# Performance work log

Measured on AMD Instinct MI355X. Metric: run time of the kernel, lower is better.

## Reference

```python
import jax, jax.numpy as jnp
import numpy as np

DIM = 64
D_STATE = 64          # = d_inner // 2, required for consistency
D_CONV = 4
EXPAND = 2
D_INNER = EXPAND * DIM  # 128
BATCH = 2
SEQ = 2048


def setup_inputs() -> dict:
    key = jax.random.key(0)
    k0, k1, k2, k3, k4, k5 = jax.random.split(key, 6)
    return {
        "x": jax.random.normal(k0, (BATCH, SEQ, DIM), jnp.float32),
        # torch nn.Linear weight layout: (out_features, in_features)
        "W_proj": jax.random.normal(k1, (3 * D_INNER, DIM), jnp.float32) / np.sqrt(DIM),
        # torch depthwise Conv1d weight layout: (d_inner, 1, d_conv)
        "conv_w": jax.random.normal(k2, (D_INNER, 1, D_CONV), jnp.float32) / np.sqrt(D_CONV),
        "conv_b": jax.random.normal(k3, (D_INNER,), jnp.float32) * 0.01,
        # negative A so exp(delta * rowsum(A)) is a stable decay (<1)
        "A": -jnp.abs(jax.random.normal(k4, (D_STATE, D_STATE), jnp.float32)) * 0.1,
        "D": jax.random.normal(k5, (D_INNER,), jnp.float32),
    }


def _scan_dir(A_bar, bx, reverse):
    # A_bar, bx: (B, L, n, d). Linear recurrence h_t = A_t * h_{t-1} + bx_t.
    A_t = jnp.moveaxis(A_bar, 1, 0)  # (L, B, n, d)
    b_t = jnp.moveaxis(bx, 1, 0)
    h0 = jnp.zeros(A_t.shape[1:], A_t.dtype)

    def step(h, inp):
        a, b = inp
        h = a * h + b
        return h, h

    _, hs = jax.lax.scan(step, h0, (A_t, b_t), reverse=reverse)
    return jnp.moveaxis(hs, 0, 1)  # (B, L, n, d)


def _forward(x, W_proj, conv_w, conv_b, A, D):
    d_inner = D.shape[0]
    n = A.shape[0]
    k = conv_w.shape[-1]

    xp = x @ W_proj.T                                   # (B, L, 3*d_inner)
    x_c_in, delta_raw, BC = jnp.split(xp, [d_inner, 2 * d_inner], axis=-1)

    # causal depthwise conv1d (torch pads d_conv-1 both sides then slices [:L])
    xc = jnp.swapaxes(x_c_in, 1, 2)                     # (B, d, L)
    xc = jax.lax.conv_general_dilated(
        xc, conv_w, window_strides=(1,), padding=[(k - 1, 0)],
        dimension_numbers=("NCH", "OIH", "NCH"), feature_group_count=d_inner)
    xc = xc + conv_b[None, :, None]
    x_conv = jnp.swapaxes(xc, 1, 2)                     # (B, L, d_inner)

    delta = jax.nn.sigmoid(delta_raw)                   # (B, L, d_inner)
    B_in, C_in = BC[..., :n], BC[..., n:]               # (B, L, n) each

    a = A.sum(axis=1)                                   # 'ij->i' contraction, (n,)
    # A_bar[b,l,n,d] = exp(delta[b,l,d] * a[n])
    A_bar = jnp.exp(delta[:, :, None, :] * a[None, None, :, None])
    # (delta*B) * x, broadcast into (B, L, n, d)
    bx = (delta * x_conv)[:, :, None, :] * B_in[..., None]

    h = _scan_dir(A_bar, bx, False) + _scan_dir(A_bar, bx, True)  # (B,L,n,d)

    y = jnp.einsum("blnd,bln->bld", h, C_in) + D * x_conv
    return y


def reference(x, W_proj, conv_w, conv_b, A, D):
    return _forward(x, W_proj, conv_w, conv_b, A, D)
```

## Files before the change

### kernel.cpp

```cpp
#include <hip/hip_runtime.h>

#define BB   2
#define TT   2048
#define DIN  128
#define NS   64
#define CL   16
#define NC   128
#define NSUP 16
#define SUPW 8
#define NP   32
#define L2E  1.4426950408889634f

#if __has_builtin(__builtin_amdgcn_exp2f)
__device__ __forceinline__ float fexp2(float x) { return __builtin_amdgcn_exp2f(x); }
#else
__device__ __forceinline__ float fexp2(float x) { return exp2f(x); }
#endif

__device__ __forceinline__ unsigned int f2bf(float f) {
  unsigned int u = __float_as_uint(f);
  u += 0x7FFFu + ((u >> 16) & 1u);
  return u >> 16;
}
__device__ __forceinline__ unsigned int packbf2(float a, float b) {
  return f2bf(a) | (f2bf(b) << 16);
}
__device__ __forceinline__ float bflo(unsigned int u) { return __uint_as_float(u << 16); }
__device__ __forceinline__ float bfhi(unsigned int u) { return __uint_as_float(u & 0xFFFF0000u); }

__global__ __launch_bounds__(128) void k_proj(
    const float* __restrict__ x, const float* __restrict__ W,
    const float* __restrict__ A,
    float* __restrict__ xcin, float* __restrict__ delta,
    float* __restrict__ Bb, float* __restrict__ Cb, float* __restrict__ a2g) {
  __shared__ float xs[128 * 65];
  int tile = blockIdx.x, rg = blockIdx.y, tid = threadIdx.x;
  int base = tile * 128;
  const float4* __restrict__ x4 = (const float4*)(x + (size_t)base * 64);
  for (int i = tid; i < 128 * 16; i += 128) {
    float4 v = x4[i];
    int row = i >> 4, c4 = (i & 15) << 2;
    xs[row * 65 + c4 + 0] = v.x;
    xs[row * 65 + c4 + 1] = v.y;
    xs[row * 65 + c4 + 2] = v.z;
    xs[row * 65 + c4 + 3] = v.w;
  }
  if (tile == 0 && rg == 0 && tid < NS) {
    float s = 0.f;
    for (int m = 0; m < NS; ++m) s += A[tid * NS + m];
    a2g[tid] = s * L2E;
  }
  __syncthreads();
  float xr[64];
#pragma unroll
  for (int k = 0; k < 64; ++k) xr[k] = xs[tid * 65 + k];
  int bt = base + tid;
#pragma unroll 4
  for (int rr = 0; rr < 16; ++rr) {
    int r = rg * 16 + rr;
    const float* __restrict__ wrow = W + r * 64;
    float a0 = 0.f, a1 = 0.f, a2 = 0.f, a3 = 0.f;
#pragma unroll
    for (int k = 0; k < 64; k += 4) {
      a0 = fmaf(xr[k + 0], wrow[k + 0], a0);
      a1 = fmaf(xr[k + 1], wrow[k + 1], a1);
      a2 = fmaf(xr[k + 2], wrow[k + 2], a2);
      a3 = fmaf(xr[k + 3], wrow[k + 3], a3);
    }
    float acc = (a0 + a1) + (a2 + a3);
    if (r < 128) {
      xcin[(size_t)bt * DIN + r] = acc;
    } else if (r < 256) {
      delta[(size_t)bt * DIN + (r - 128)] = 1.f / (1.f + fexp2(-acc * L2E));
    } else if (r < 320) {
      Bb[(size_t)bt * NS + (r - 256)] = acc;
    } else {
      Cb[(size_t)bt * NS + (r - 320)] = acc;
    }
  }
}

__global__ __launch_bounds__(1024) void k_scan1(
    const float* __restrict__ xcin, const float* __restrict__ delta,
    const float* __restrict__ Bb, const float* __restrict__ a2g,
    const float* __restrict__ cw, const float* __restrict__ cb,
    unsigned int* __restrict__ hendP, float* __restrict__ sumd) {
  __shared__ float xcs[(CL + 3) * DIN];
  __shared__ float des[CL * DIN];
  __shared__ float Bs[CL * NS];
  int c = blockIdx.x, b = blockIdx.y;
  int tid = threadIdx.x;
  int d = tid & 127;
  int g = __builtin_amdgcn_readfirstlane(tid >> 7);
  int t0 = c * CL;
  {
    const float* __restrict__ xcB = xcin + (size_t)b * TT * DIN;
    for (int i = tid; i < (CL + 3) * 32; i += 1024) {
      int row = i >> 5, c4 = i & 31;
      int t = t0 - 3 + row;
      float4 v = make_float4(0.f, 0.f, 0.f, 0.f);
      if (t >= 0) v = ((const float4*)(xcB + (size_t)t * DIN))[c4];
      ((float4*)xcs)[i] = v;
    }
    if (tid < CL * 32)
      ((float4*)des)[tid] = ((const float4*)(delta + (size_t)(b * TT + t0) * DIN))[tid];
    if (tid < CL * 16)
      ((float4*)Bs)[tid] = ((const float4*)(Bb + (size_t)(b * TT + t0) * NS))[tid];
  }
  float cw0 = cw[d * 4 + 0], cw1 = cw[d * 4 + 1], cw2 = cw[d * 4 + 2], cw3 = cw[d * 4 + 3];
  float cbd = cb[d];
  int nb = g * 8;
  float a2r[8];
#pragma unroll
  for (int j = 0; j < 8; ++j) a2r[j] = a2g[nb + j];
  __syncthreads();
  float hf[8], hr[8], Pp[8];
#pragma unroll
  for (int j = 0; j < 8; ++j) { hf[j] = 0.f; hr[j] = 0.f; Pp[j] = 1.f; }
  float sd = 0.f;
  float w0 = xcs[0 * DIN + d], w1 = xcs[1 * DIN + d], w2 = xcs[2 * DIN + d];
#pragma unroll
  for (int i = 0; i < CL; ++i) {
    float w3 = xcs[(i + 3) * DIN + d];
    float xconv = fmaf(cw0, w0, fmaf(cw1, w1, fmaf(cw2, w2, fmaf(cw3, w3, cbd))));
    float de = des[i * DIN + d];
    sd += de;
    float dxv = de * xconv;
#pragma unroll
    for (int jq = 0; jq < 2; ++jq) {
      float4 bq = *(const float4*)&Bs[i * NS + nb + jq * 4];
      float b0 = dxv * bq.x, b1 = dxv * bq.y, b2 = dxv * bq.z, b3 = dxv * bq.w;
      float e0 = fexp2(de * a2r[jq * 4 + 0]);
      float e1 = fexp2(de * a2r[jq * 4 + 1]);
      float e2 = fexp2(de * a2r[jq * 4 + 2]);
      float e3 = fexp2(de * a2r[jq * 4 + 3]);
      hf[jq * 4 + 0] = fmaf(e0, hf[jq * 4 + 0], b0);
      hr[jq * 4 + 0] = fmaf(Pp[jq * 4 + 0], b0, hr[jq * 4 + 0]); Pp[jq * 4 + 0] *= e0;
      hf[jq * 4 + 1] = fmaf(e1, hf[jq * 4 + 1], b1);
      hr[jq * 4 + 1] = fmaf(Pp[jq * 4 + 1], b1, hr[jq * 4 + 1]); Pp[jq * 4 + 1] *= e1;
      hf[jq * 4 + 2] = fmaf(e2, hf[jq * 4 + 2], b2);
      hr[jq * 4 + 2] = fmaf(Pp[jq * 4 + 2], b2, hr[jq * 4 + 2]); Pp[jq * 4 + 2] *= e2;
      hf[jq * 4 + 3] = fmaf(e3, hf[jq * 4 + 3], b3);
      hr[jq * 4 + 3] = fmaf(Pp[jq * 4 + 3], b3, hr[jq * 4 + 3]); Pp[jq * 4 + 3] *= e3;
    }
    w0 = w1; w1 = w2; w2 = w3;
  }
  size_t h0 = (((size_t)(0 * NC + c) * BB + b) * NP + (nb >> 1)) * DIN + d;
  size_t h1 = (((size_t)(1 * NC + c) * BB + b) * NP + (nb >> 1)) * DIN + d;
#pragma unroll
  for (int jp = 0; jp < 4; ++jp) {
    hendP[h0 + (size_t)jp * DIN] = packbf2(hf[2 * jp], hf[2 * jp + 1]);
    hendP[h1 + (size_t)jp * DIN] = packbf2(hr[2 * jp], hr[2 * jp + 1]);
  }
  if (g == 0) sumd[(c * BB + b) * DIN + d] = sd;
}

__global__ __launch_bounds__(512) void k_comb2A(
    const unsigned int* __restrict__ hendP, unsigned int* __restrict__ hinLP,
    const float* __restrict__ sumd, const float* __restrict__ a2g,
    float* __restrict__ S, float* __restrict__ sumdS,
    float* __restrict__ sumdPf, float* __restrict__ sumdPr) {
  int idx = blockIdx.x * 512 + threadIdx.x;
  int dd = idx & 127;
  int np = (idx >> 7) & 31;
  int sp = (idx >> 12) & 15;
  int bd = idx >> 16;
  int b = bd >> 1, dir = bd & 1;
  int n0 = 2 * np, n1 = 2 * np + 1;
  float a2n0 = a2g[n0], a2n1 = a2g[n1];
  float sd[SUPW];
  unsigned int hv[SUPW];
#pragma unroll
  for (int k = 0; k < SUPW; ++k) {
    int kk = dir ? (SUPW - 1 - k) : k;
    int cc = sp * SUPW + kk;
    sd[k] = sumd[(cc * BB + b) * DIN + dd];
    hv[k] = hendP[(((size_t)(dir * NC + cc) * BB + b) * NP + np) * DIN + dd];
  }
  if (np == 0) {
    float running = 0.f;
#pragma unroll
    for (int k = 0; k < SUPW; ++k) {
      int kk = dir ? (SUPW - 1 - k) : k;
      int cc = sp * SUPW + kk;
      if (dir) sumdPr[(cc * BB + b) * DIN + dd] = running;
      else     sumdPf[(cc * BB + b) * DIN + dd] = running;
      running += sd[k];
    }
    if (dir == 0) sumdS[(sp * BB + b) * DIN + dd] = running;
  }
  float c0 = 0.f, c1 = 0.f;
#pragma unroll
  for (int k = 0; k < SUPW; ++k) {
    int kk = dir ? (SUPW - 1 - k) : k;
    int cc = sp * SUPW + kk;
    hinLP[(((size_t)(dir * NC + cc) * BB + b) * NP + np) * DIN + dd] = packbf2(c0, c1);
    float e0 = fexp2(a2n0 * sd[k]);
    float e1 = fexp2(a2n1 * sd[k]);
    c0 = fmaf(e0, c0, bflo(hv[k]));
    c1 = fmaf(e1, c1, bfhi(hv[k]));
  }
  size_t sb = ((((size_t)dir * NSUP + sp) * BB + b) * NS + n0) * DIN + dd;
  S[sb] = c0;
  S[sb + (size_t)DIN] = c1;
}

__global__ __launch_bounds__(256) void k_comb2B(
    const float* __restrict__ S, const float* __restrict__ sumdS,
    const float* __restrict__ a2g, float* __restrict__ Csup) {
  int idx = blockIdx.x * 256 + threadIdx.x;
  int dd = idx & 127;
  int n = (idx >> 7) & 63;
  int bd = idx >> 13;
  int b = bd >> 1, dir = bd & 1;
  float a2n = a2g[n];
  float sdS[NSUP], Sv[NSUP];
#pragma unroll
  for (int sp = 0; sp < NSUP; ++sp) {
    sdS[sp] = sumdS[(sp * BB + b) * DIN + dd];
    Sv[sp] = S[((((size_t)dir * NSUP + sp) * BB + b) * NS + n) * DIN + dd];
  }
  float carry = 0.f;
#pragma unroll
  for (int k = 0; k < NSUP; ++k) {
    int sp = dir ? (NSUP - 1 - k) : k;
    Csup[((((size_t)dir * NSUP + sp) * BB + b) * NS + n) * DIN + dd] = carry;
    carry = fmaf(fexp2(a2n * sdS[sp]), carry, Sv[sp]);
  }
}

__global__ __launch_bounds__(1024) void k_scan2(
    const float* __restrict__ xcin, const float* __restrict__ delta,
    const float* __restrict__ Bb, const float* __restrict__ Cb,
    const float* __restrict__ a2g, const float* __restrict__ cw,
    const float* __restrict__ cb, const float* __restrict__ Dp,
    const unsigned int* __restrict__ hinLP, const float* __restrict__ Csup,
    const float* __restrict__ sumdPf, const float* __restrict__ sumdPr,
    float* __restrict__ out) {
  __shared__ float yred[8][CL][DIN];
  int c = blockIdx.x, b = blockIdx.y;
  int tid = threadIdx.x;
  int d = tid & 127;
  int g = __builtin_amdgcn_readfirstlane(tid >> 7);
  int dir = g >> 2;
  int nb = (g & 3) * 16;
  float cw0 = cw[d * 4 + 0], cw1 = cw[d * 4 + 1], cw2 = cw[d * 4 + 2], cw3 = cw[d * 4 + 3];
  float cbd = cb[d];
  float Dd = Dp[d];
  float a2r[16];
#pragma unroll
  for (int j = 0; j < 16; ++j) a2r[j] = a2g[nb + j];
  int sp = c >> 3;
  float Sloc = dir ? sumdPr[(c * BB + b) * DIN + d] : sumdPf[(c * BB + b) * DIN + d];
  float h[16];
  size_t hb0 = (((size_t)(dir * NC + c) * BB + b) * NP + (nb >> 1)) * DIN + d;
  size_t sb0 = ((((size_t)dir * NSUP + sp) * BB + b) * NS + nb) * DIN + d;
#pragma unroll
  for (int jp = 0; jp < 8; ++jp) {
    unsigned int u = hinLP[hb0 + (size_t)jp * DIN];
    float pe0 = fexp2(a2r[2 * jp] * Sloc);
    float pe1 = fexp2(a2r[2 * jp + 1] * Sloc);
    h[2 * jp]     = fmaf(pe0, Csup[sb0 + (size_t)(2 * jp) * DIN], bflo(u));
    h[2 * jp + 1] = fmaf(pe1, Csup[sb0 + (size_t)(2 * jp + 1) * DIN], bfhi(u));
  }
  int t0 = c * CL;
  const float* __restrict__ xcB = xcin + (size_t)b * TT * DIN + d;
  const float* __restrict__ deB = delta + (size_t)b * TT * DIN + d;
  const float* __restrict__ BbB = Bb + (size_t)b * TT * NS + nb;
  const float* __restrict__ CbB = Cb + (size_t)b * TT * NS + nb;
  bool addD = (g == 0);
  float w0, w1, w2, w3;
  if (dir == 0) {
    int t = t0;
    w0 = (t - 3 >= 0) ? xcB[(t - 3) * DIN] : 0.f;
    w1 = (t - 2 >= 0) ? xcB[(t - 2) * DIN] : 0.f;
    w2 = (t - 1 >= 0) ? xcB[(t - 1) * DIN] : 0.f;
    w3 = xcB[t * DIN];
#pragma unroll
    for (int i = 0; i < CL; ++i) {
      float xconv = fmaf(cw0, w0, fmaf(cw1, w1, fmaf(cw2, w2, fmaf(cw3, w3, cbd))));
      float de = deB[t * DIN];
      float dxv = de * xconv;
      float yv = addD ? Dd * xconv : 0.f;
#pragma unroll
      for (int jq = 0; jq < 4; ++jq) {
        float4 bq = *(const float4*)&BbB[t * NS + jq * 4];
        float4 cq = *(const float4*)&CbB[t * NS + jq * 4];
        float e0 = fexp2(de * a2r[jq * 4 + 0]);
        h[jq * 4 + 0] = fmaf(e0, h[jq * 4 + 0], dxv * bq.x); yv = fmaf(h[jq * 4 + 0], cq.x, yv);
        float e1 = fexp2(de * a2r[jq * 4 + 1]);
        h[jq * 4 + 1] = fmaf(e1, h[jq * 4 + 1], dxv * bq.y); yv = fmaf(h[jq * 4 + 1], cq.y, yv);
        float e2 = fexp2(de * a2r[jq * 4 + 2]);
        h[jq * 4 + 2] = fmaf(e2, h[jq * 4 + 2], dxv * bq.z); yv = fmaf(h[jq * 4 + 2], cq.z, yv);
        float e3 = fexp2(de * a2r[jq * 4 + 3]);
        h[jq * 4 + 3] = fmaf(e3, h[jq * 4 + 3], dxv * bq.w); yv = fmaf(h[jq * 4 + 3], cq.w, yv);
      }
      yred[g][i][d] = yv;
      if (i < CL - 1) { ++t; w0 = w1; w1 = w2; w2 = w3; w3 = xcB[t * DIN]; }
    }
  } else {
    int t = t0 + CL - 1;
    w3 = xcB[t * DIN];
    w2 = xcB[(t - 1) * DIN];
    w1 = xcB[(t - 2) * DIN];
    w0 = xcB[(t - 3) * DIN];
#pragma unroll
    for (int i = 0; i < CL; ++i) {
      float xconv = fmaf(cw0, w0, fmaf(cw1, w1, fmaf(cw2, w2, fmaf(cw3, w3, cbd))));
      float de = deB[t * DIN];
      float dxv = de * xconv;
      float yv = 0.f;
#pragma unroll
      for (int jq = 0; jq < 4; ++jq) {
        float4 bq = *(const float4*)&BbB[t * NS + jq * 4];
        float4 cq = *(const float4*)&CbB[t * NS + jq * 4];
        float e0 = fexp2(de * a2r[jq * 4 + 0]);
        h[jq * 4 + 0] = fmaf(e0, h[jq * 4 + 0], dxv * bq.x); yv = fmaf(h[jq * 4 + 0], cq.x, yv);
        float e1 = fexp2(de * a2r[jq * 4 + 1]);
        h[jq * 4 + 1] = fmaf(e1, h[jq * 4 + 1], dxv * bq.y); yv = fmaf(h[jq * 4 + 1], cq.y, yv);
        float e2 = fexp2(de * a2r[jq * 4 + 2]);
        h[jq * 4 + 2] = fmaf(e2, h[jq * 4 + 2], dxv * bq.z); yv = fmaf(h[jq * 4 + 2], cq.z, yv);
        float e3 = fexp2(de * a2r[jq * 4 + 3]);
        h[jq * 4 + 3] = fmaf(e3, h[jq * 4 + 3], dxv * bq.w); yv = fmaf(h[jq * 4 + 3], cq.w, yv);
      }
      yred[g][i][d] = yv;
      if (i < CL - 1) { --t; w3 = w2; w2 = w1; w1 = w0; w0 = (t - 3 >= 0) ? xcB[(t - 3) * DIN] : 0.f; }
    }
  }
  __syncthreads();
#pragma unroll
  for (int k = 0; k < 2; ++k) {
    int p = k * 1024 + tid;
    int i = p >> 7, d2 = p & 127;
    int ir = CL - 1 - i;
    float sf = (yred[0][i][d2] + yred[1][i][d2]) + (yred[2][i][d2] + yred[3][i][d2]);
    float sr = (yred[4][ir][d2] + yred[5][ir][d2]) + (yred[6][ir][d2] + yred[7][ir][d2]);
    out[((size_t)b * TT + t0 + i) * DIN + d2] = sf + sr;
  }
}

extern "C" void kernel_launch(void* const* d_in, const int* in_sizes, int n_in,
                              void* d_out, int out_size, void* d_ws, size_t ws_size,
                              hipStream_t stream) {
  const float* x  = (const float*)d_in[0];
  const float* W  = (const float*)d_in[1];
  const float* cw = (const float*)d_in[2];
  const float* cb = (const float*)d_in[3];
  const float* A  = (const float*)d_in[4];
  const float* Dp = (const float*)d_in[5];
  float* out = (float*)d_out;

  float* ws = (float*)d_ws;
  float* xcin   = ws;
  float* delta  = xcin + 524288;
  float* Bbuf   = delta + 524288;
  float* Cbuf   = Bbuf + 262144;
  float* a2g    = Cbuf + 262144;
  float* sumd   = a2g + 128;
  float* sumdPf = sumd + 32768;
  float* sumdPr = sumdPf + 32768;
  float* sumdS  = sumdPr + 32768;
  float* Sb     = sumdS + 4096;
  float* Csup   = Sb + 524288;
  unsigned int* hendP = (unsigned int*)(Csup + 524288);
  unsigned int* hinLP = hendP + 2097152;

  hipLaunchKernelGGL(k_proj,   dim3(32, 24), dim3(128), 0, stream,
                     x, W, A, xcin, delta, Bbuf, Cbuf, a2g);
  hipLaunchKernelGGL(k_scan1,  dim3(NC, BB), dim3(1024), 0, stream,
                     xcin, delta, Bbuf, a2g, cw, cb, hendP, sumd);
  hipLaunchKernelGGL(k_comb2A, dim3(512), dim3(512), 0, stream,
                     hendP, hinLP, sumd, a2g, Sb, sumdS, sumdPf, sumdPr);
  hipLaunchKernelGGL(k_comb2B, dim3(128), dim3(256), 0, stream,
                     Sb, sumdS, a2g, Csup);
  hipLaunchKernelGGL(k_scan2,  dim3(NC, BB), dim3(1024), 0, stream,
                     xcin, delta, Bbuf, Cbuf, a2g, cw, cb, Dp, hinLP, Csup,
                     sumdPf, sumdPr, out);
}
```

Baseline: 62.96 us.

## Recompute intra-superchunk carry in scan2 instead of storing hinLP; split proj tiles

Drops the hinLP buffer that k_comb2A wrote and k_scan2 read. k_scan2 now rebuilds the within-superchunk incoming state itself by walking up to seven preceding chunk-end states from hendP, then adds the superchunk carry. This saves a large bf16 write and read pass but adds redundant exp and FMA work and serial loads inside scan2, with uneven work across chunks. Separately, k_proj now uses 64-row tiles with each half of the block computing 8 output rows, which doubles the grid.

```diff
diff --git a/kernel.cpp b/kernel.cpp
--- a/kernel.cpp
+++ b/kernel.cpp
@@ -33,11 +33,11 @@
     const float* __restrict__ A,
     float* __restrict__ xcin, float* __restrict__ delta,
     float* __restrict__ Bb, float* __restrict__ Cb, float* __restrict__ a2g) {
-  __shared__ float xs[128 * 65];
+  __shared__ float xs[64 * 65];
   int tile = blockIdx.x, rg = blockIdx.y, tid = threadIdx.x;
-  int base = tile * 128;
+  int base = tile * 64;
   const float4* __restrict__ x4 = (const float4*)(x + (size_t)base * 64);
-  for (int i = tid; i < 128 * 16; i += 128) {
+  for (int i = tid; i < 64 * 16; i += 128) {
     float4 v = x4[i];
     int row = i >> 4, c4 = (i & 15) << 2;
     xs[row * 65 + c4 + 0] = v.x;
@@ -51,13 +51,14 @@
     a2g[tid] = s * L2E;
   }
   __syncthreads();
+  int tl = tid & 63, half = tid >> 6;
   float xr[64];
 #pragma unroll
-  for (int k = 0; k < 64; ++k) xr[k] = xs[tid * 65 + k];
-  int bt = base + tid;
+  for (int k = 0; k < 64; ++k) xr[k] = xs[tl * 65 + k];
+  int bt = base + tl;
 #pragma unroll 4
-  for (int rr = 0; rr < 16; ++rr) {
-    int r = rg * 16 + rr;
+  for (int rr = 0; rr < 8; ++rr) {
+    int r = rg * 16 + half * 8 + rr;
     const float* __restrict__ wrow = W + r * 64;
     float a0 = 0.f, a1 = 0.f, a2 = 0.f, a3 = 0.f;
 #pragma unroll
@@ -156,7 +157,7 @@
 }
 
 __global__ __launch_bounds__(512) void k_comb2A(
-    const unsigned int* __restrict__ hendP, unsigned int* __restrict__ hinLP,
+    const unsigned int* __restrict__ hendP,
     const float* __restrict__ sumd, const float* __restrict__ a2g,
     float* __restrict__ S, float* __restrict__ sumdS,
     float* __restrict__ sumdPf, float* __restrict__ sumdPr) {
@@ -192,9 +193,6 @@
   float c0 = 0.f, c1 = 0.f;
 #pragma unroll
   for (int k = 0; k < SUPW; ++k) {
-    int kk = dir ? (SUPW - 1 - k) : k;
-    int cc = sp * SUPW + kk;
-    hinLP[(((size_t)(dir * NC + cc) * BB + b) * NP + np) * DIN + dd] = packbf2(c0, c1);
     float e0 = fexp2(a2n0 * sd[k]);
     float e1 = fexp2(a2n1 * sd[k]);
     c0 = fmaf(e0, c0, bflo(hv[k]));
@@ -234,7 +232,8 @@
     const float* __restrict__ Bb, const float* __restrict__ Cb,
     const float* __restrict__ a2g, const float* __restrict__ cw,
     const float* __restrict__ cb, const float* __restrict__ Dp,
-    const unsigned int* __restrict__ hinLP, const float* __restrict__ Csup,
+    const unsigned int* __restrict__ hendP, const float* __restrict__ sumd,
+    const float* __restrict__ Csup,
     const float* __restrict__ sumdPf, const float* __restrict__ sumdPr,
     float* __restrict__ out) {
   __shared__ float yred[8][CL][DIN];
@@ -253,15 +252,40 @@
   int sp = c >> 3;
   float Sloc = dir ? sumdPr[(c * BB + b) * DIN + d] : sumdPf[(c * BB + b) * DIN + d];
   float h[16];
-  size_t hb0 = (((size_t)(dir * NC + c) * BB + b) * NP + (nb >> 1)) * DIN + d;
+#pragma unroll
+  for (int j = 0; j < 16; ++j) h[j] = 0.f;
+  if (dir == 0) {
+    for (int kc = sp * 8; kc < c; ++kc) {
+      float sdv = sumd[(kc * BB + b) * DIN + d];
+      size_t hb = (((size_t)(0 * NC + kc) * BB + b) * NP + (nb >> 1)) * DIN + d;
+#pragma unroll
+      for (int jp = 0; jp < 8; ++jp) {
+        unsigned int u = hendP[hb + (size_t)jp * DIN];
+        float e0 = fexp2(a2r[2 * jp] * sdv);
+        float e1 = fexp2(a2r[2 * jp + 1] * sdv);
+        h[2 * jp]     = fmaf(e0, h[2 * jp], bflo(u));
+        h[2 * jp + 1] = fmaf(e1, h[2 * jp + 1], bfhi(u));
+      }
+    }
+  } else {
+    for (int kc = sp * 8 + 7; kc > c; --kc) {
+      float sdv = sumd[(kc * BB + b) * DIN + d];
+      size_t hb = (((size_t)(1 * NC + kc) * BB + b) * NP + (nb >> 1)) * DIN + d;
+#pragma unroll
+      for (int jp = 0; jp < 8; ++jp) {
+        unsigned int u = hendP[hb + (size_t)jp * DIN];
+        float e0 = fexp2(a2r[2 * jp] * sdv);
+        float e1 = fexp2(a2r[2 * jp + 1] * sdv);
+        h[2 * jp]     = fmaf(e0, h[2 * jp], bflo(u));
+        h[2 * jp + 1] = fmaf(e1, h[2 * jp + 1], bfhi(u));
+      }
+    }
+  }
   size_t sb0 = ((((size_t)dir * NSUP + sp) * BB + b) * NS + nb) * DIN + d;
 #pragma unroll
-  for (int jp = 0; jp < 8; ++jp) {
-    unsigned int u = hinLP[hb0 + (size_t)jp * DIN];
-    float pe0 = fexp2(a2r[2 * jp] * Sloc);
-    float pe1 = fexp2(a2r[2 * jp + 1] * Sloc);
-    h[2 * jp]     = fmaf(pe0, Csup[sb0 + (size_t)(2 * jp) * DIN], bflo(u));
-    h[2 * jp + 1] = fmaf(pe1, Csup[sb0 + (size_t)(2 * jp + 1) * DIN], bfhi(u));
+  for (int j = 0; j < 16; ++j) {
+    float pe = fexp2(a2r[j] * Sloc);
+    h[j] = fmaf(pe, Csup[sb0 + (size_t)j * DIN], h[j]);
   }
   int t0 = c * CL;
   const float* __restrict__ xcB = xcin + (size_t)b * TT * DIN + d;
@@ -363,17 +387,16 @@
   float* Sb     = sumdS + 4096;
   float* Csup   = Sb + 524288;
   unsigned int* hendP = (unsigned int*)(Csup + 524288);
-  unsigned int* hinLP = hendP + 2097152;
-
-  hipLaunchKernelGGL(k_proj,   dim3(32, 24), dim3(128), 0, stream,
+
+  hipLaunchKernelGGL(k_proj,   dim3(64, 24), dim3(128), 0, stream,
                      x, W, A, xcin, delta, Bbuf, Cbuf, a2g);
   hipLaunchKernelGGL(k_scan1,  dim3(NC, BB), dim3(1024), 0, stream,
                      xcin, delta, Bbuf, a2g, cw, cb, hendP, sumd);
   hipLaunchKernelGGL(k_comb2A, dim3(512), dim3(512), 0, stream,
-                     hendP, hinLP, sumd, a2g, Sb, sumdS, sumdPf, sumdPr);
+                     hendP, sumd, a2g, Sb, sumdS, sumdPf, sumdPr);
   hipLaunchKernelGGL(k_comb2B, dim3(128), dim3(256), 0, stream,
                      Sb, sumdS, a2g, Csup);
   hipLaunchKernelGGL(k_scan2,  dim3(NC, BB), dim3(1024), 0, stream,
-                     xcin, delta, Bbuf, Cbuf, a2g, cw, cb, Dp, hinLP, Csup,
+                     xcin, delta, Bbuf, Cbuf, a2g, cw, cb, Dp, hendP, sumd, Csup,
                      sumdPf, sumdPr, out);
 }
```

New measurement: 67.41 us. 7.1% more time.

## Fuse two-level chunk carry combine into one kernel writing final carries

Applied to the files above, without the earlier changes.

Merges the two combine kernels into one block-per-(batch,dir,state-pair) kernel. It computes superchunk partial carries, runs the cross-superchunk scan in shared memory, then writes fully resolved bf16 initial states per chunk. The second scan kernel therefore no longer reads Csup and the prefix sums or evaluates extra exponentials at start. This removes one launch and several intermediate global buffers. The cost is only 128 blocks and a serial 16-step section run by one warp group, plus re-quantising the combined state to bf16.

```diff
diff --git a/kernel.cpp b/kernel.cpp
--- a/kernel.cpp
+++ b/kernel.cpp
@@ -155,77 +155,67 @@
   if (g == 0) sumd[(c * BB + b) * DIN + d] = sd;
 }
 
-__global__ __launch_bounds__(512) void k_comb2A(
-    const unsigned int* __restrict__ hendP, unsigned int* __restrict__ hinLP,
-    const float* __restrict__ sumd, const float* __restrict__ a2g,
-    float* __restrict__ S, float* __restrict__ sumdS,
-    float* __restrict__ sumdPf, float* __restrict__ sumdPr) {
-  int idx = blockIdx.x * 512 + threadIdx.x;
-  int dd = idx & 127;
-  int np = (idx >> 7) & 31;
-  int sp = (idx >> 12) & 15;
-  int bd = idx >> 16;
-  int b = bd >> 1, dir = bd & 1;
-  int n0 = 2 * np, n1 = 2 * np + 1;
-  float a2n0 = a2g[n0], a2n1 = a2g[n1];
-  float sd[SUPW];
-  unsigned int hv[SUPW];
-#pragma unroll
-  for (int k = 0; k < SUPW; ++k) {
-    int kk = dir ? (SUPW - 1 - k) : k;
-    int cc = sp * SUPW + kk;
-    sd[k] = sumd[(cc * BB + b) * DIN + dd];
-    hv[k] = hendP[(((size_t)(dir * NC + cc) * BB + b) * NP + np) * DIN + dd];
-  }
-  if (np == 0) {
-    float running = 0.f;
+__global__ __launch_bounds__(1024) void k_comb(
+    const unsigned int* __restrict__ hendP, const float* __restrict__ sumd,
+    const float* __restrict__ a2g, unsigned int* __restrict__ hinP) {
+  __shared__ float S0[NSUP][DIN], S1[NSUP][DIN];
+  __shared__ float sdS[NSUP][DIN];
+  __shared__ float C0[NSUP][DIN], C1[NSUP][DIN];
+  int bid = blockIdx.x;
+  int np = bid & 31;
+  int dirb = bid >> 5;
+  int dir = dirb & 1, b = dirb >> 1;
+  int tid = threadIdx.x;
+  int d = tid & 127;
+  int sl = __builtin_amdgcn_readfirstlane(tid >> 7);
+  float a2n0 = a2g[2 * np], a2n1 = a2g[2 * np + 1];
+  float hinLo0[2][SUPW], hinLo1[2][SUPW], pfLoc[2][SUPW];
+#pragma unroll
+  for (int ss = 0; ss < 2; ++ss) {
+    int sp = sl + ss * 8;
+    float c0 = 0.f, c1 = 0.f, pf = 0.f;
 #pragma unroll
     for (int k = 0; k < SUPW; ++k) {
-      int kk = dir ? (SUPW - 1 - k) : k;
-      int cc = sp * SUPW + kk;
-      if (dir) sumdPr[(cc * BB + b) * DIN + dd] = running;
-      else     sumdPf[(cc * BB + b) * DIN + dd] = running;
-      running += sd[k];
-    }
-    if (dir == 0) sumdS[(sp * BB + b) * DIN + dd] = running;
-  }
-  float c0 = 0.f, c1 = 0.f;
-#pragma unroll
-  for (int k = 0; k < SUPW; ++k) {
-    int kk = dir ? (SUPW - 1 - k) : k;
-    int cc = sp * SUPW + kk;
-    hinLP[(((size_t)(dir * NC + cc) * BB + b) * NP + np) * DIN + dd] = packbf2(c0, c1);
-    float e0 = fexp2(a2n0 * sd[k]);
-    float e1 = fexp2(a2n1 * sd[k]);
-    c0 = fmaf(e0, c0, bflo(hv[k]));
-    c1 = fmaf(e1, c1, bfhi(hv[k]));
-  }
-  size_t sb = ((((size_t)dir * NSUP + sp) * BB + b) * NS + n0) * DIN + dd;
-  S[sb] = c0;
-  S[sb + (size_t)DIN] = c1;
-}
-
-__global__ __launch_bounds__(256) void k_comb2B(
-    const float* __restrict__ S, const float* __restrict__ sumdS,
-    const float* __restrict__ a2g, float* __restrict__ Csup) {
-  int idx = blockIdx.x * 256 + threadIdx.x;
-  int dd = idx & 127;
-  int n = (idx >> 7) & 63;
-  int bd = idx >> 13;
-  int b = bd >> 1, dir = bd & 1;
-  float a2n = a2g[n];
-  float sdS[NSUP], Sv[NSUP];
-#pragma unroll
-  for (int sp = 0; sp < NSUP; ++sp) {
-    sdS[sp] = sumdS[(sp * BB + b) * DIN + dd];
-    Sv[sp] = S[((((size_t)dir * NSUP + sp) * BB + b) * NS + n) * DIN + dd];
-  }
-  float carry = 0.f;
-#pragma unroll
-  for (int k = 0; k < NSUP; ++k) {
-    int sp = dir ? (NSUP - 1 - k) : k;
-    Csup[((((size_t)dir * NSUP + sp) * BB + b) * NS + n) * DIN + dd] = carry;
-    carry = fmaf(fexp2(a2n * sdS[sp]), carry, Sv[sp]);
+      int cc = sp * SUPW + (dir ? (SUPW - 1 - k) : k);
+      float sdv = sumd[(cc * BB + b) * DIN + d];
+      unsigned int hv = hendP[(((size_t)(dir * NC + cc) * BB + b) * NP + np) * DIN + d];
+      hinLo0[ss][k] = c0; hinLo1[ss][k] = c1; pfLoc[ss][k] = pf;
+      float e0 = fexp2(a2n0 * sdv);
+      float e1 = fexp2(a2n1 * sdv);
+      c0 = fmaf(e0, c0, bflo(hv));
+      c1 = fmaf(e1, c1, bfhi(hv));
+      pf += sdv;
+    }
+    S0[sp][d] = c0; S1[sp][d] = c1; sdS[sp][d] = pf;
+  }
+  __syncthreads();
+  if (sl == 0) {
+    float c0 = 0.f, c1 = 0.f;
+#pragma unroll
+    for (int k = 0; k < NSUP; ++k) {
+      int sp = dir ? (NSUP - 1 - k) : k;
+      C0[sp][d] = c0; C1[sp][d] = c1;
+      float sv = sdS[sp][d];
+      float e0 = fexp2(a2n0 * sv);
+      float e1 = fexp2(a2n1 * sv);
+      c0 = fmaf(e0, c0, S0[sp][d]);
+      c1 = fmaf(e1, c1, S1[sp][d]);
+    }
+  }
+  __syncthreads();
+#pragma unroll
+  for (int ss = 0; ss < 2; ++ss) {
+    int sp = sl + ss * 8;
+    float cs0 = C0[sp][d], cs1 = C1[sp][d];
+#pragma unroll
+    for (int k = 0; k < SUPW; ++k) {
+      int cc = sp * SUPW + (dir ? (SUPW - 1 - k) : k);
+      float pe0 = fexp2(a2n0 * pfLoc[ss][k]);
+      float pe1 = fexp2(a2n1 * pfLoc[ss][k]);
+      float v0 = fmaf(pe0, cs0, hinLo0[ss][k]);
+      float v1 = fmaf(pe1, cs1, hinLo1[ss][k]);
+      hinP[(((size_t)(dir * NC + cc) * BB + b) * NP + np) * DIN + d] = packbf2(v0, v1);
+    }
   }
 }
 
@@ -234,8 +224,7 @@
     const float* __restrict__ Bb, const float* __restrict__ Cb,
     const float* __restrict__ a2g, const float* __restrict__ cw,
     const float* __restrict__ cb, const float* __restrict__ Dp,
-    const unsigned int* __restrict__ hinLP, const float* __restrict__ Csup,
-    const float* __restrict__ sumdPf, const float* __restrict__ sumdPr,
+    const unsigned int* __restrict__ hinP,
     float* __restrict__ out) {
   __shared__ float yred[8][CL][DIN];
   int c = blockIdx.x, b = blockIdx.y;
@@ -250,18 +239,13 @@
   float a2r[16];
 #pragma unroll
   for (int j = 0; j < 16; ++j) a2r[j] = a2g[nb + j];
-  int sp = c >> 3;
-  float Sloc = dir ? sumdPr[(c * BB + b) * DIN + d] : sumdPf[(c * BB + b) * DIN + d];
   float h[16];
   size_t hb0 = (((size_t)(dir * NC + c) * BB + b) * NP + (nb >> 1)) * DIN + d;
-  size_t sb0 = ((((size_t)dir * NSUP + sp) * BB + b) * NS + nb) * DIN + d;
 #pragma unroll
   for (int jp = 0; jp < 8; ++jp) {
-    unsigned int u = hinLP[hb0 + (size_t)jp * DIN];
-    float pe0 = fexp2(a2r[2 * jp] * Sloc);
-    float pe1 = fexp2(a2r[2 * jp + 1] * Sloc);
-    h[2 * jp]     = fmaf(pe0, Csup[sb0 + (size_t)(2 * jp) * DIN], bflo(u));
-    h[2 * jp + 1] = fmaf(pe1, Csup[sb0 + (size_t)(2 * jp + 1) * DIN], bfhi(u));
+    unsigned int u = hinP[hb0 + (size_t)jp * DIN];
+    h[2 * jp]     = bflo(u);
+    h[2 * jp + 1] = bfhi(u);
   }
   int t0 = c * CL;
   const float* __restrict__ xcB = xcin + (size_t)b * TT * DIN + d;
@@ -357,23 +341,15 @@
   float* Cbuf   = Bbuf + 262144;
   float* a2g    = Cbuf + 262144;
   float* sumd   = a2g + 128;
-  float* sumdPf = sumd + 32768;
-  float* sumdPr = sumdPf + 32768;
-  float* sumdS  = sumdPr + 32768;
-  float* Sb     = sumdS + 4096;
-  float* Csup   = Sb + 524288;
-  unsigned int* hendP = (unsigned int*)(Csup + 524288);
-  unsigned int* hinLP = hendP + 2097152;
-
-  hipLaunchKernelGGL(k_proj,   dim3(32, 24), dim3(128), 0, stream,
+  unsigned int* hendP = (unsigned int*)(sumd + 32768);
+  unsigned int* hinP  = hendP + 2097152;
+
+  hipLaunchKernelGGL(k_proj,  dim3(32, 24), dim3(128), 0, stream,
                      x, W, A, xcin, delta, Bbuf, Cbuf, a2g);
-  hipLaunchKernelGGL(k_scan1,  dim3(NC, BB), dim3(1024), 0, stream,
+  hipLaunchKernelGGL(k_scan1, dim3(NC, BB), dim3(1024), 0, stream,
                      xcin, delta, Bbuf, a2g, cw, cb, hendP, sumd);
-  hipLaunchKernelGGL(k_comb2A, dim3(512), dim3(512), 0, stream,
-                     hendP, hinLP, sumd, a2g, Sb, sumdS, sumdPf, sumdPr);
-  hipLaunchKernelGGL(k_comb2B, dim3(128), dim3(256), 0, stream,
-                     Sb, sumdS, a2g, Csup);
-  hipLaunchKernelGGL(k_scan2,  dim3(NC, BB), dim3(1024), 0, stream,
-                     xcin, delta, Bbuf, Cbuf, a2g, cw, cb, Dp, hinLP, Csup,
-                     sumdPf, sumdPr, out);
-}
+  hipLaunchKernelGGL(k_comb,  dim3(128), dim3(1024), 0, stream,
+                     hendP, sumd, a2g, hinP);
+  hipLaunchKernelGGL(k_scan2, dim3(NC, BB), dim3(1024), 0, stream,
+                     xcin, delta, Bbuf, Cbuf, a2g, cw, cb, Dp, hinP, out);
+}
```

Measured after the change: 65.20 us. 3.6% more time.

## Split state dimension across two blocks in scan kernels with atomic output accumulation

Applied to the files above, without the earlier changes.

The scan1 and scan2 kernels now use a third grid dimension that splits the 64 state channels into two halves. Each thread carries fewer registers and the grid has twice as many blocks. scan2 accumulates its partial outputs with atomic adds into an output buffer that comb2B zero-fills beforehand. k_proj is also regridded to 8 rows per block with full unrolling. This raises parallelism and occupancy, at the cost of recomputing the conv and staged loads per half and adding atomic traffic on the output.

```diff
diff --git a/kernel.cpp b/kernel.cpp
--- a/kernel.cpp
+++ b/kernel.cpp
@@ -17,13 +17,13 @@
 __device__ __forceinline__ float fexp2(float x) { return exp2f(x); }
 #endif
 
-__device__ __forceinline__ unsigned int f2bf(float f) {
+__device__ __forceinline__ unsigned int f2bfu(float f) {
   unsigned int u = __float_as_uint(f);
   u += 0x7FFFu + ((u >> 16) & 1u);
   return u >> 16;
 }
 __device__ __forceinline__ unsigned int packbf2(float a, float b) {
-  return f2bf(a) | (f2bf(b) << 16);
+  return f2bfu(a) | (f2bfu(b) << 16);
 }
 __device__ __forceinline__ float bflo(unsigned int u) { return __uint_as_float(u << 16); }
 __device__ __forceinline__ float bfhi(unsigned int u) { return __uint_as_float(u & 0xFFFF0000u); }
@@ -55,9 +55,9 @@
 #pragma unroll
   for (int k = 0; k < 64; ++k) xr[k] = xs[tid * 65 + k];
   int bt = base + tid;
-#pragma unroll 4
-  for (int rr = 0; rr < 16; ++rr) {
-    int r = rg * 16 + rr;
+#pragma unroll
+  for (int rr = 0; rr < 8; ++rr) {
+    int r = rg * 8 + rr;
     const float* __restrict__ wrow = W + r * 64;
     float a0 = 0.f, a1 = 0.f, a2 = 0.f, a3 = 0.f;
 #pragma unroll
@@ -88,7 +88,7 @@
   __shared__ float xcs[(CL + 3) * DIN];
   __shared__ float des[CL * DIN];
   __shared__ float Bs[CL * NS];
-  int c = blockIdx.x, b = blockIdx.y;
+  int c = blockIdx.x, b = blockIdx.y, z = blockIdx.z;
   int tid = threadIdx.x;
   int d = tid & 127;
   int g = __builtin_amdgcn_readfirstlane(tid >> 7);
@@ -109,14 +109,14 @@
   }
   float cw0 = cw[d * 4 + 0], cw1 = cw[d * 4 + 1], cw2 = cw[d * 4 + 2], cw3 = cw[d * 4 + 3];
   float cbd = cb[d];
-  int nb = g * 8;
-  float a2r[8];
-#pragma unroll
-  for (int j = 0; j < 8; ++j) a2r[j] = a2g[nb + j];
+  int nb = z * 32 + g * 4;
+  float a2r[4];
+#pragma unroll
+  for (int j = 0; j < 4; ++j) a2r[j] = a2g[nb + j];
   __syncthreads();
-  float hf[8], hr[8], Pp[8];
-#pragma unroll
-  for (int j = 0; j < 8; ++j) { hf[j] = 0.f; hr[j] = 0.f; Pp[j] = 1.f; }
+  float hf[4], hr[4], Pp[4];
+#pragma unroll
+  for (int j = 0; j < 4; ++j) { hf[j] = 0.f; hr[j] = 0.f; Pp[j] = 1.f; }
   float sd = 0.f;
   float w0 = xcs[0 * DIN + d], w1 = xcs[1 * DIN + d], w2 = xcs[2 * DIN + d];
 #pragma unroll
@@ -126,33 +126,26 @@
     float de = des[i * DIN + d];
     sd += de;
     float dxv = de * xconv;
-#pragma unroll
-    for (int jq = 0; jq < 2; ++jq) {
-      float4 bq = *(const float4*)&Bs[i * NS + nb + jq * 4];
-      float b0 = dxv * bq.x, b1 = dxv * bq.y, b2 = dxv * bq.z, b3 = dxv * bq.w;
-      float e0 = fexp2(de * a2r[jq * 4 + 0]);
-      float e1 = fexp2(de * a2r[jq * 4 + 1]);
-      float e2 = fexp2(de * a2r[jq * 4 + 2]);
-      float e3 = fexp2(de * a2r[jq * 4 + 3]);
-      hf[jq * 4 + 0] = fmaf(e0, hf[jq * 4 + 0], b0);
-      hr[jq * 4 + 0] = fmaf(Pp[jq * 4 + 0], b0, hr[jq * 4 + 0]); Pp[jq * 4 + 0] *= e0;
-      hf[jq * 4 + 1] = fmaf(e1, hf[jq * 4 + 1], b1);
-      hr[jq * 4 + 1] = fmaf(Pp[jq * 4 + 1], b1, hr[jq * 4 + 1]); Pp[jq * 4 + 1] *= e1;
-      hf[jq * 4 + 2] = fmaf(e2, hf[jq * 4 + 2], b2);
-      hr[jq * 4 + 2] = fmaf(Pp[jq * 4 + 2], b2, hr[jq * 4 + 2]); Pp[jq * 4 + 2] *= e2;
-      hf[jq * 4 + 3] = fmaf(e3, hf[jq * 4 + 3], b3);
-      hr[jq * 4 + 3] = fmaf(Pp[jq * 4 + 3], b3, hr[jq * 4 + 3]); Pp[jq * 4 + 3] *= e3;
-    }
+    float4 bq = *(const float4*)&Bs[i * NS + nb];
+    float b0 = dxv * bq.x, b1 = dxv * bq.y, b2 = dxv * bq.z, b3 = dxv * bq.w;
+    float e0 = fexp2(de * a2r[0]);
+    float e1 = fexp2(de * a2r[1]);
+    float e2 = fexp2(de * a2r[2]);
+    float e3 = fexp2(de * a2r[3]);
+    hf[0] = fmaf(e0, hf[0], b0); hr[0] = fmaf(Pp[0], b0, hr[0]); Pp[0] *= e0;
+    hf[1] = fmaf(e1, hf[1], b1); hr[1] = fmaf(Pp[1], b1, hr[1]); Pp[1] *= e1;
+    hf[2] = fmaf(e2, hf[2], b2); hr[2] = fmaf(Pp[2], b2, hr[2]); Pp[2] *= e2;
+    hf[3] = fmaf(e3, hf[3], b3); hr[3] = fmaf(Pp[3], b3, hr[3]); Pp[3] *= e3;
     w0 = w1; w1 = w2; w2 = w3;
   }
   size_t h0 = (((size_t)(0 * NC + c) * BB + b) * NP + (nb >> 1)) * DIN + d;
   size_t h1 = (((size_t)(1 * NC + c) * BB + b) * NP + (nb >> 1)) * DIN + d;
 #pragma unroll
-  for (int jp = 0; jp < 4; ++jp) {
+  for (int jp = 0; jp < 2; ++jp) {
     hendP[h0 + (size_t)jp * DIN] = packbf2(hf[2 * jp], hf[2 * jp + 1]);
     hendP[h1 + (size_t)jp * DIN] = packbf2(hr[2 * jp], hr[2 * jp + 1]);
   }
-  if (g == 0) sumd[(c * BB + b) * DIN + d] = sd;
+  if (z == 0 && g == 0) sumd[(c * BB + b) * DIN + d] = sd;
 }
 
 __global__ __launch_bounds__(512) void k_comb2A(
@@ -207,7 +200,8 @@
 
 __global__ __launch_bounds__(256) void k_comb2B(
     const float* __restrict__ S, const float* __restrict__ sumdS,
-    const float* __restrict__ a2g, float* __restrict__ Csup) {
+    const float* __restrict__ a2g, float* __restrict__ Csup,
+    float* __restrict__ out) {
   int idx = blockIdx.x * 256 + threadIdx.x;
   int dd = idx & 127;
   int n = (idx >> 7) & 63;
@@ -227,6 +221,10 @@
     Csup[((((size_t)dir * NSUP + sp) * BB + b) * NS + n) * DIN + dd] = carry;
     carry = fmaf(fexp2(a2n * sdS[sp]), carry, Sv[sp]);
   }
+  float4 z4 = make_float4(0.f, 0.f, 0.f, 0.f);
+  float4* __restrict__ o4 = (float4*)out;
+#pragma unroll
+  for (int q = 0; q < 4; ++q) o4[(size_t)idx * 4 + q] = z4;
 }
 
 __global__ __launch_bounds__(1024) void k_scan2(
@@ -238,25 +236,25 @@
     const float* __restrict__ sumdPf, const float* __restrict__ sumdPr,
     float* __restrict__ out) {
   __shared__ float yred[8][CL][DIN];
-  int c = blockIdx.x, b = blockIdx.y;
+  int c = blockIdx.x, b = blockIdx.y, z = blockIdx.z;
   int tid = threadIdx.x;
   int d = tid & 127;
   int g = __builtin_amdgcn_readfirstlane(tid >> 7);
   int dir = g >> 2;
-  int nb = (g & 3) * 16;
+  int nb = z * 32 + (g & 3) * 8;
   float cw0 = cw[d * 4 + 0], cw1 = cw[d * 4 + 1], cw2 = cw[d * 4 + 2], cw3 = cw[d * 4 + 3];
   float cbd = cb[d];
   float Dd = Dp[d];
-  float a2r[16];
-#pragma unroll
-  for (int j = 0; j < 16; ++j) a2r[j] = a2g[nb + j];
+  float a2r[8];
+#pragma unroll
+  for (int j = 0; j < 8; ++j) a2r[j] = a2g[nb + j];
   int sp = c >> 3;
   float Sloc = dir ? sumdPr[(c * BB + b) * DIN + d] : sumdPf[(c * BB + b) * DIN + d];
-  float h[16];
+  float h[8];
   size_t hb0 = (((size_t)(dir * NC + c) * BB + b) * NP + (nb >> 1)) * DIN + d;
   size_t sb0 = ((((size_t)dir * NSUP + sp) * BB + b) * NS + nb) * DIN + d;
 #pragma unroll
-  for (int jp = 0; jp < 8; ++jp) {
+  for (int jp = 0; jp < 4; ++jp) {
     unsigned int u = hinLP[hb0 + (size_t)jp * DIN];
     float pe0 = fexp2(a2r[2 * jp] * Sloc);
     float pe1 = fexp2(a2r[2 * jp + 1] * Sloc);
@@ -268,7 +266,7 @@
   const float* __restrict__ deB = delta + (size_t)b * TT * DIN + d;
   const float* __restrict__ BbB = Bb + (size_t)b * TT * NS + nb;
   const float* __restrict__ CbB = Cb + (size_t)b * TT * NS + nb;
-  bool addD = (g == 0);
+  bool addD = (g == 0) && (z == 0);
   float w0, w1, w2, w3;
   if (dir == 0) {
     int t = t0;
@@ -283,7 +281,7 @@
       float dxv = de * xconv;
       float yv = addD ? Dd * xconv : 0.f;
 #pragma unroll
-      for (int jq = 0; jq < 4; ++jq) {
+      for (int jq = 0; jq < 2; ++jq) {
         float4 bq = *(const float4*)&BbB[t * NS + jq * 4];
         float4 cq = *(const float4*)&CbB[t * NS + jq * 4];
         float e0 = fexp2(de * a2r[jq * 4 + 0]);
@@ -311,7 +309,7 @@
       float dxv = de * xconv;
       float yv = 0.f;
 #pragma unroll
-      for (int jq = 0; jq < 4; ++jq) {
+      for (int jq = 0; jq < 2; ++jq) {
         float4 bq = *(const float4*)&BbB[t * NS + jq * 4];
         float4 cq = *(const float4*)&CbB[t * NS + jq * 4];
         float e0 = fexp2(de * a2r[jq * 4 + 0]);
@@ -335,7 +333,7 @@
     int ir = CL - 1 - i;
     float sf = (yred[0][i][d2] + yred[1][i][d2]) + (yred[2][i][d2] + yred[3][i][d2]);
     float sr = (yred[4][ir][d2] + yred[5][ir][d2]) + (yred[6][ir][d2] + yred[7][ir][d2]);
-    out[((size_t)b * TT + t0 + i) * DIN + d2] = sf + sr;
+    unsafeAtomicAdd(&out[((size_t)b * TT + t0 + i) * DIN + d2], sf + sr);
   }
 }
 
@@ -365,15 +363,15 @@
   unsigned int* hendP = (unsigned int*)(Csup + 524288);
   unsigned int* hinLP = hendP + 2097152;
 
-  hipLaunchKernelGGL(k_proj,   dim3(32, 24), dim3(128), 0, stream,
+  hipLaunchKernelGGL(k_proj,   dim3(32, 48), dim3(128), 0, stream,
                      x, W, A, xcin, delta, Bbuf, Cbuf, a2g);
-  hipLaunchKernelGGL(k_scan1,  dim3(NC, BB), dim3(1024), 0, stream,
+  hipLaunchKernelGGL(k_scan1,  dim3(NC, BB, 2), dim3(1024), 0, stream,
                      xcin, delta, Bbuf, a2g, cw, cb, hendP, sumd);
   hipLaunchKernelGGL(k_comb2A, dim3(512), dim3(512), 0, stream,
                      hendP, hinLP, sumd, a2g, Sb, sumdS, sumdPf, sumdPr);
   hipLaunchKernelGGL(k_comb2B, dim3(128), dim3(256), 0, stream,
-                     Sb, sumdS, a2g, Csup);
-  hipLaunchKernelGGL(k_scan2,  dim3(NC, BB), dim3(1024), 0, stream,
+                     Sb, sumdS, a2g, Csup, out);
+  hipLaunchKernelGGL(k_scan2,  dim3(NC, BB, 2), dim3(1024), 0, stream,
                      xcin, delta, Bbuf, Cbuf, a2g, cw, cb, Dp, hinLP, Csup,
                      sumdPf, sumdPr, out);
 }
```

New measurement: 65.63 us. 4.2% more time.
